# Kernel tuning notes

Hardware: AMD Instinct MI355X
Metric: run time of the kernel (lower is better)

## Reference

```python
import jax, jax.numpy as jnp
import numpy as np

T, H, F, E, K = 1024, 1024, 2048, 8, 2  # tokens, hidden, ffn_inter, experts, top_k


def setup_inputs() -> dict:
    key = jax.random.key(0)
    ks = jax.random.split(key, 7)
    return {
        "hidden_states": jax.random.normal(ks[0], (T, H), dtype=jnp.float32),
        "token_selected_experts": jax.random.randint(ks[1], (T, K), 0, E, dtype=jnp.int32),
        "token_final_scales": jax.random.uniform(ks[2], (T, K), dtype=jnp.float32),
        "w1": jax.random.normal(ks[3], (E, 2 * F, H), dtype=jnp.float32) * 0.02,  # gated fc1: [gate; linear]
        "b1": jax.random.normal(ks[4], (E, 2 * F), dtype=jnp.float32) * 0.02,
        "w2": jax.random.normal(ks[5], (E, H, F), dtype=jnp.float32) * 0.02,
        "b2": jax.random.normal(ks[6], (E, H), dtype=jnp.float32) * 0.02,
    }


def reference(hidden_states, token_selected_experts, token_final_scales, w1, b1, w2, b2):
    # Grouped GEMM fc1 over all experts: [T, E, 2F]
    h1 = jnp.einsum('th,efh->tef', hidden_states, w1) + b1[None]
    ffn = w2.shape[2]
    gate, lin = h1[..., :ffn], h1[..., ffn:]
    act = jax.nn.silu(gate) * lin                      # swiglu gated activation, [T, E, F]
    y_all = jnp.einsum('tef,ehf->teh', act, w2) + b2[None]  # fc2, [T, E, H]
    # Gather the top-k selected experts per token and combine with final scales
    sel = token_selected_experts.astype(jnp.int32)     # [T, K]
    y_sel = jnp.take_along_axis(y_all, sel[:, :, None], axis=1)  # [T, K, H]
    out = jnp.sum(y_sel * token_final_scales[:, :, None], axis=1)  # [T, H]
    return out
```

## Files before the change

### kernel.cpp

```cpp
#include <hip/hip_runtime.h>
#include <hip/hip_bf16.h>
#include <cstdint>
#include <cstddef>

#define TDIM 1024
#define HDIM 1024
#define FDIM 2048
#define NEXP 8
#define NENT 2048

typedef __bf16 bf16_t;
typedef __bf16 bf16x4 __attribute__((ext_vector_type(4)));
typedef __bf16 bf16x8 __attribute__((ext_vector_type(8)));
typedef float  f32x4  __attribute__((ext_vector_type(4)));

#define H_ELEMS ((size_t)TDIM*HDIM)

#define WB_OFFSETS 0
#define WB_ETOK    64
#define WB_ESCALE  (WB_ETOK + NENT*4)
#define WB_ACT     16512
#define WB_H       (WB_ACT + (size_t)NENT*FDIM*2)

__device__ __forceinline__ void gload16(const void* g, void* l) {
  __builtin_amdgcn_global_load_lds((const __attribute__((address_space(1))) void*)g,
                                   (__attribute__((address_space(3))) void*)l, 16, 0, 0);
}

__global__ void route_all(const int* __restrict__ sel, const float* __restrict__ scal,
                          int* __restrict__ offsets, int* __restrict__ etok,
                          float* __restrict__ escale) {
  __shared__ int cnt[NEXP], cnt2[NEXP], offs[NEXP+1];
  const int t = threadIdx.x;
  if (t < NEXP) { cnt[t] = 0; cnt2[t] = 0; }
  __syncthreads();
  int e8[8];
  #pragma unroll
  for (int q = 0; q < 8; q++) {
    int i = t*8 + q;
    e8[q] = sel[i];
    atomicAdd(&cnt[e8[q]], 1);
  }
  __syncthreads();
  if (t == 0) {
    int s = 0;
    for (int e = 0; e < NEXP; e++) { offs[e] = s; offsets[e] = s; s += cnt[e]; }
    offs[NEXP] = s; offsets[NEXP] = s;
  }
  __syncthreads();
  #pragma unroll
  for (int q = 0; q < 8; q++) {
    int i = t*8 + q;
    int e = e8[q];
    int pos = offs[e] + atomicAdd(&cnt2[e], 1);
    etok[pos]   = i >> 1;
    escale[pos] = scal[i];
  }
}

__global__ void convert_h(const float* __restrict__ h, bf16_t* __restrict__ hbf) {
  size_t idx = ((size_t)blockIdx.x*256 + threadIdx.x) * 8;
  float4 v0 = ((const float4*)(h + idx))[0];
  float4 v1 = ((const float4*)(h + idx))[1];
  bf16x8 o;
  o[0]=(bf16_t)v0.x; o[1]=(bf16_t)v0.y; o[2]=(bf16_t)v0.z; o[3]=(bf16_t)v0.w;
  o[4]=(bf16_t)v1.x; o[5]=(bf16_t)v1.y; o[6]=(bf16_t)v1.z; o[7]=(bf16_t)v1.w;
  *(bf16x8*)(hbf + idx) = o;
}


__global__ __launch_bounds__(512, 4) void gemm1_v3(
    const bf16_t* __restrict__ hbf, const float* __restrict__ w1,
    const float* __restrict__ b1, const int* __restrict__ offsets,
    const int* __restrict__ etok, bf16_t* __restrict__ act)
{
  const int e   = blockIdx.z;
  const int off = offsets[e];
  const int nt  = offsets[e+1] - off;
  const int m0  = blockIdx.y * 128;
  if (m0 >= nt) return;
  const int n0  = blockIdx.x * 64;

  __shared__ __align__(16) bf16_t As[2][128*32];
  __shared__ __align__(16) bf16_t Bg[64*32];
  __shared__ __align__(16) bf16_t Bl[64*32];

  const int tid  = threadIdx.x;
  const int w    = tid >> 6, lane = tid & 63;
  const int quad = lane >> 4, lr = lane & 15;
  const int wm   = w >> 1,  wn = w & 1;

  const int ar   = w*16 + (lane >> 2);
  const int aseg = (lane & 3) ^ (ar & 3);
  int ent = m0 + ar; if (ent > nt-1) ent = nt-1;
  const int tok = etok[off + ent];
  const bf16_t* asrc = hbf + (size_t)tok*HDIM + aseg*8;
  bf16_t* adst[2] = { &As[0][w*512], &As[1][w*512] };

  const int tr = tid >> 3, c4 = tid & 7;
  const float* gsrc = w1 + ((size_t)e*2*FDIM + (size_t)(n0 + tr))*HDIM + c4*4;
  const float* lsrc = gsrc + (size_t)FDIM*HDIM;
  const int bofs = tr*32 + (((c4 >> 1) ^ (tr & 3)) << 3) + (c4 & 1)*4;

  f32x4 accg[2][2] = {}, accl[2][2] = {};

  gload16(asrc, adst[0]);
  float4 g4 = *(const float4*)gsrc;
  float4 l4 = *(const float4*)lsrc;

  int p = 0;
  for (int k0 = 0; k0 < HDIM; k0 += 32, p ^= 1) {
    __syncthreads();
    {
      bf16x4 v;
      v[0]=(bf16_t)g4.x; v[1]=(bf16_t)g4.y; v[2]=(bf16_t)g4.z; v[3]=(bf16_t)g4.w;
      *(bf16x4*)&Bg[bofs] = v;
      v[0]=(bf16_t)l4.x; v[1]=(bf16_t)l4.y; v[2]=(bf16_t)l4.z; v[3]=(bf16_t)l4.w;
      *(bf16x4*)&Bl[bofs] = v;
    }
    if (k0 + 32 < HDIM) {
      gload16(asrc + k0 + 32, adst[p^1]);
      g4 = *(const float4*)(gsrc + k0 + 32);
      l4 = *(const float4*)(lsrc + k0 + 32);
    }
    __syncthreads();

    bf16x8 af[2], gf[2], lf[2];
    #pragma unroll
    for (int i = 0; i < 2; i++) {
      const int m = wm*32 + i*16 + lr;
      af[i] = *(const bf16x8*)&As[p][m*32 + ((quad ^ (m & 3)) << 3)];
    }
    #pragma unroll
    for (int j = 0; j < 2; j++) {
      const int n = wn*32 + j*16 + lr;
      gf[j] = *(const bf16x8*)&Bg[n*32 + ((quad ^ (n & 3)) << 3)];
      lf[j] = *(const bf16x8*)&Bl[n*32 + ((quad ^ (n & 3)) << 3)];
    }
    #pragma unroll
    for (int i = 0; i < 2; i++)
      #pragma unroll
      for (int j = 0; j < 2; j++) {
        accg[i][j] = __builtin_amdgcn_mfma_f32_16x16x32_bf16(af[i], gf[j], accg[i][j], 0, 0, 0);
        accl[i][j] = __builtin_amdgcn_mfma_f32_16x16x32_bf16(af[i], lf[j], accl[i][j], 0, 0, 0);
      }
  }

  #pragma unroll
  for (int j = 0; j < 2; j++) {
    const int f = n0 + wn*32 + j*16 + lr;
    const float bg_ = b1[e*2*FDIM + f];
    const float bl_ = b1[e*2*FDIM + FDIM + f];
    #pragma unroll
    for (int i = 0; i < 2; i++) {
      #pragma unroll
      for (int r = 0; r < 4; r++) {
        const int m = wm*32 + i*16 + quad*4 + r;
        if (m0 + m < nt) {
          const float g = accg[i][j][r] + bg_;
          const float l = accl[i][j][r] + bl_;
          const float s = g / (1.f + __expf(-g)) * l;
          act[(size_t)(off + m0 + m)*FDIM + f] = (bf16_t)s;
        }
      }
    }
  }
}

__global__ __launch_bounds__(512, 4) void gemm2_v3(
    const bf16_t* __restrict__ act, const float* __restrict__ w2,
    const float* __restrict__ b2, const int* __restrict__ offsets,
    const int* __restrict__ etok, const float* __restrict__ escale,
    float* __restrict__ out)
{
  const int e   = blockIdx.z;
  const int off = offsets[e];
  const int nt  = offsets[e+1] - off;
  const int m0  = blockIdx.y * 128;
  if (m0 >= nt) return;
  const int n0  = (blockIdx.x >> 1) * 64;
  const int kc  = blockIdx.x & 1;
  const int kbeg = kc * (FDIM/2);

  __shared__ __align__(16) bf16_t As[2][128*32];
  __shared__ __align__(16) bf16_t Bs[64*32];

  const int tid  = threadIdx.x;
  const int w    = tid >> 6, lane = tid & 63;
  const int quad = lane >> 4, lr = lane & 15;
  const int wm   = w >> 1,  wn = w & 1;

  const int ar   = w*16 + (lane >> 2);
  const int aseg = (lane & 3) ^ (ar & 3);
  int ent = m0 + ar; if (ent > nt-1) ent = nt-1;
  const bf16_t* asrc = act + (size_t)(off + ent)*FDIM + kbeg + aseg*8;
  bf16_t* adst[2] = { &As[0][w*512], &As[1][w*512] };

  const int tr = tid >> 3, c4 = tid & 7;
  const float* bsrc = w2 + ((size_t)e*HDIM + (size_t)(n0 + tr))*FDIM + kbeg + c4*4;
  const int bofs = tr*32 + (((c4 >> 1) ^ (tr & 3)) << 3) + (c4 & 1)*4;

  f32x4 acc[2][2] = {};

  gload16(asrc, adst[0]);
  float4 b4 = *(const float4*)bsrc;

  int p = 0;
  for (int k0 = 0; k0 < FDIM/2; k0 += 32, p ^= 1) {
    __syncthreads();
    {
      bf16x4 v;
      v[0]=(bf16_t)b4.x; v[1]=(bf16_t)b4.y; v[2]=(bf16_t)b4.z; v[3]=(bf16_t)b4.w;
      *(bf16x4*)&Bs[bofs] = v;
    }
    if (k0 + 32 < FDIM/2) {
      gload16(asrc + k0 + 32, adst[p^1]);
      b4 = *(const float4*)(bsrc + k0 + 32);
    }
    __syncthreads();

    bf16x8 af[2], bfr[2];
    #pragma unroll
    for (int i = 0; i < 2; i++) {
      const int m = wm*32 + i*16 + lr;
      af[i] = *(const bf16x8*)&As[p][m*32 + ((quad ^ (m & 3)) << 3)];
    }
    #pragma unroll
    for (int j = 0; j < 2; j++) {
      const int n = wn*32 + j*16 + lr;
      bfr[j] = *(const bf16x8*)&Bs[n*32 + ((quad ^ (n & 3)) << 3)];
    }
    #pragma unroll
    for (int i = 0; i < 2; i++)
      #pragma unroll
      for (int j = 0; j < 2; j++)
        acc[i][j] = __builtin_amdgcn_mfma_f32_16x16x32_bf16(af[i], bfr[j], acc[i][j], 0, 0, 0);
  }

  #pragma unroll
  for (int i = 0; i < 2; i++) {
    #pragma unroll
    for (int r = 0; r < 4; r++) {
      const int m = wm*32 + i*16 + quad*4 + r;
      if (m0 + m < nt) {
        const int slot = off + m0 + m;
        const int t    = etok[slot];
        const float s  = escale[slot];
        #pragma unroll
        for (int j = 0; j < 2; j++) {
          const int n = n0 + wn*32 + j*16 + lr;
          float v = acc[i][j][r];
          if (kc == 0) v += b2[e*HDIM + n];
          atomicAdd(&out[(size_t)t*HDIM + n], s * v);
        }
      }
    }
  }
}

extern "C" void kernel_launch(void* const* d_in, const int* in_sizes, int n_in,
                              void* d_out, int out_size, void* d_ws, size_t ws_size,
                              hipStream_t stream) {
  const float* hidden = (const float*)d_in[0];
  const int*   sel    = (const int*)d_in[1];
  const float* scal   = (const float*)d_in[2];
  const float* w1     = (const float*)d_in[3];
  const float* b1     = (const float*)d_in[4];
  const float* w2     = (const float*)d_in[5];
  const float* b2     = (const float*)d_in[6];
  float* out = (float*)d_out;

  char* ws = (char*)d_ws;
  int*    offsets = (int*)(ws + WB_OFFSETS);
  int*    etok    = (int*)(ws + WB_ETOK);
  float*  escale  = (float*)(ws + WB_ESCALE);
  bf16_t* act     = (bf16_t*)(ws + WB_ACT);
  bf16_t* hbf     = (bf16_t*)(ws + WB_H);

  hipMemsetAsync(d_out, 0, (size_t)out_size * sizeof(float), stream);

  route_all<<<1, 256, 0, stream>>>(sel, scal, offsets, etok, escale);
  convert_h<<<(int)(H_ELEMS/8/256), 256, 0, stream>>>(hidden, hbf);

  gemm1_v3<<<dim3(FDIM/64, NENT/128, NEXP), 512, 0, stream>>>(hbf, w1, b1, offsets, etok, act);
  gemm2_v3<<<dim3((HDIM/64)*2, NENT/128, NEXP), 512, 0, stream>>>(act, w2, b2, offsets, etok, escale, out);
}
```

Before: 346.6 us.

## Drop LDS staging in MoE GEMMs and load MFMA fragments directly from global

Both grouped GEMM kernels stop staging A and B tiles through shared memory. Each lane now reads its MFMA fragments straight from global memory and converts fp32 weights to bf16 in registers. The M tile shrinks from 128 to 64 rows and blocks from 512 to 256 threads, so more blocks launch. This removes the barriers and LDS traffic, but loses cross-wave reuse: each wave re-reads weights and activations from global, and a lane's 32-byte row slices are not coalesced, so memory traffic goes up.

```diff
diff --git a/kernel.cpp b/kernel.cpp
--- a/kernel.cpp
+++ b/kernel.cpp
@@ -21,11 +21,6 @@
 #define WB_ESCALE  (WB_ETOK + NENT*4)
 #define WB_ACT     16512
 #define WB_H       (WB_ACT + (size_t)NENT*FDIM*2)
-
-__device__ __forceinline__ void gload16(const void* g, void* l) {
-  __builtin_amdgcn_global_load_lds((const __attribute__((address_space(1))) void*)g,
-                                   (__attribute__((address_space(3))) void*)l, 16, 0, 0);
-}
 
 __global__ void route_all(const int* __restrict__ sel, const float* __restrict__ scal,
                           int* __restrict__ offsets, int* __restrict__ etok,
@@ -68,8 +63,15 @@
   *(bf16x8*)(hbf + idx) = o;
 }
 
-
-__global__ __launch_bounds__(512, 4) void gemm1_v3(
+__device__ __forceinline__ bf16x8 cvt8(const float4 a, const float4 b) {
+  bf16x8 o;
+  o[0]=(bf16_t)a.x; o[1]=(bf16_t)a.y; o[2]=(bf16_t)a.z; o[3]=(bf16_t)a.w;
+  o[4]=(bf16_t)b.x; o[5]=(bf16_t)b.y; o[6]=(bf16_t)b.z; o[7]=(bf16_t)b.w;
+  return o;
+}
+
+
+__global__ __launch_bounds__(256, 4) void gemm1_v4(
     const bf16_t* __restrict__ hbf, const float* __restrict__ w1,
     const float* __restrict__ b1, const int* __restrict__ offsets,
     const int* __restrict__ etok, bf16_t* __restrict__ act)
@@ -77,65 +79,47 @@
   const int e   = blockIdx.z;
   const int off = offsets[e];
   const int nt  = offsets[e+1] - off;
-  const int m0  = blockIdx.y * 128;
+  const int m0  = blockIdx.y * 64;
   if (m0 >= nt) return;
   const int n0  = blockIdx.x * 64;
-
-  __shared__ __align__(16) bf16_t As[2][128*32];
-  __shared__ __align__(16) bf16_t Bg[64*32];
-  __shared__ __align__(16) bf16_t Bl[64*32];
 
   const int tid  = threadIdx.x;
   const int w    = tid >> 6, lane = tid & 63;
   const int quad = lane >> 4, lr = lane & 15;
   const int wm   = w >> 1,  wn = w & 1;
 
-  const int ar   = w*16 + (lane >> 2);
-  const int aseg = (lane & 3) ^ (ar & 3);
-  int ent = m0 + ar; if (ent > nt-1) ent = nt-1;
-  const int tok = etok[off + ent];
-  const bf16_t* asrc = hbf + (size_t)tok*HDIM + aseg*8;
-  bf16_t* adst[2] = { &As[0][w*512], &As[1][w*512] };
-
-  const int tr = tid >> 3, c4 = tid & 7;
-  const float* gsrc = w1 + ((size_t)e*2*FDIM + (size_t)(n0 + tr))*HDIM + c4*4;
-  const float* lsrc = gsrc + (size_t)FDIM*HDIM;
-  const int bofs = tr*32 + (((c4 >> 1) ^ (tr & 3)) << 3) + (c4 & 1)*4;
+  const bf16_t* aptr[2];
+  #pragma unroll
+  for (int i = 0; i < 2; i++) {
+    int ent = m0 + wm*32 + i*16 + lr;
+    if (ent > nt-1) ent = nt-1;
+    const int tok = etok[off + ent];
+    aptr[i] = hbf + (size_t)tok*HDIM + quad*8;
+  }
+  const float* gptr[2];
+  const float* lptr[2];
+  #pragma unroll
+  for (int j = 0; j < 2; j++) {
+    const int n = n0 + wn*32 + j*16 + lr;
+    gptr[j] = w1 + ((size_t)e*2*FDIM + n)*HDIM + quad*8;
+    lptr[j] = gptr[j] + (size_t)FDIM*HDIM;
+  }
 
   f32x4 accg[2][2] = {}, accl[2][2] = {};
 
-  gload16(asrc, adst[0]);
-  float4 g4 = *(const float4*)gsrc;
-  float4 l4 = *(const float4*)lsrc;
-
-  int p = 0;
-  for (int k0 = 0; k0 < HDIM; k0 += 32, p ^= 1) {
-    __syncthreads();
-    {
-      bf16x4 v;
-      v[0]=(bf16_t)g4.x; v[1]=(bf16_t)g4.y; v[2]=(bf16_t)g4.z; v[3]=(bf16_t)g4.w;
-      *(bf16x4*)&Bg[bofs] = v;
-      v[0]=(bf16_t)l4.x; v[1]=(bf16_t)l4.y; v[2]=(bf16_t)l4.z; v[3]=(bf16_t)l4.w;
-      *(bf16x4*)&Bl[bofs] = v;
-    }
-    if (k0 + 32 < HDIM) {
-      gload16(asrc + k0 + 32, adst[p^1]);
-      g4 = *(const float4*)(gsrc + k0 + 32);
-      l4 = *(const float4*)(lsrc + k0 + 32);
-    }
-    __syncthreads();
-
+  for (int k0 = 0; k0 < HDIM; k0 += 32) {
     bf16x8 af[2], gf[2], lf[2];
     #pragma unroll
-    for (int i = 0; i < 2; i++) {
-      const int m = wm*32 + i*16 + lr;
-      af[i] = *(const bf16x8*)&As[p][m*32 + ((quad ^ (m & 3)) << 3)];
-    }
+    for (int i = 0; i < 2; i++)
+      af[i] = *(const bf16x8*)(aptr[i] + k0);
     #pragma unroll
     for (int j = 0; j < 2; j++) {
-      const int n = wn*32 + j*16 + lr;
-      gf[j] = *(const bf16x8*)&Bg[n*32 + ((quad ^ (n & 3)) << 3)];
-      lf[j] = *(const bf16x8*)&Bl[n*32 + ((quad ^ (n & 3)) << 3)];
+      const float4* gp = (const float4*)(gptr[j] + k0);
+      const float4* lp = (const float4*)(lptr[j] + k0);
+      float4 ga = gp[0], gb = gp[1];
+      float4 la = lp[0], lb = lp[1];
+      gf[j] = cvt8(ga, gb);
+      lf[j] = cvt8(la, lb);
     }
     #pragma unroll
     for (int i = 0; i < 2; i++)
@@ -167,7 +151,7 @@
   }
 }
 
-__global__ __launch_bounds__(512, 4) void gemm2_v3(
+__global__ __launch_bounds__(256, 4) void gemm2_v4(
     const bf16_t* __restrict__ act, const float* __restrict__ w2,
     const float* __restrict__ b2, const int* __restrict__ offsets,
     const int* __restrict__ etok, const float* __restrict__ escale,
@@ -176,59 +160,43 @@
   const int e   = blockIdx.z;
   const int off = offsets[e];
   const int nt  = offsets[e+1] - off;
-  const int m0  = blockIdx.y * 128;
+  const int m0  = blockIdx.y * 64;
   if (m0 >= nt) return;
   const int n0  = (blockIdx.x >> 1) * 64;
   const int kc  = blockIdx.x & 1;
   const int kbeg = kc * (FDIM/2);
 
-  __shared__ __align__(16) bf16_t As[2][128*32];
-  __shared__ __align__(16) bf16_t Bs[64*32];
-
   const int tid  = threadIdx.x;
   const int w    = tid >> 6, lane = tid & 63;
   const int quad = lane >> 4, lr = lane & 15;
   const int wm   = w >> 1,  wn = w & 1;
 
-  const int ar   = w*16 + (lane >> 2);
-  const int aseg = (lane & 3) ^ (ar & 3);
-  int ent = m0 + ar; if (ent > nt-1) ent = nt-1;
-  const bf16_t* asrc = act + (size_t)(off + ent)*FDIM + kbeg + aseg*8;
-  bf16_t* adst[2] = { &As[0][w*512], &As[1][w*512] };
-
-  const int tr = tid >> 3, c4 = tid & 7;
-  const float* bsrc = w2 + ((size_t)e*HDIM + (size_t)(n0 + tr))*FDIM + kbeg + c4*4;
-  const int bofs = tr*32 + (((c4 >> 1) ^ (tr & 3)) << 3) + (c4 & 1)*4;
+  const bf16_t* aptr[2];
+  #pragma unroll
+  for (int i = 0; i < 2; i++) {
+    int ent = m0 + wm*32 + i*16 + lr;
+    if (ent > nt-1) ent = nt-1;
+    aptr[i] = act + (size_t)(off + ent)*FDIM + kbeg + quad*8;
+  }
+  const float* bptr[2];
+  #pragma unroll
+  for (int j = 0; j < 2; j++) {
+    const int n = n0 + wn*32 + j*16 + lr;
+    bptr[j] = w2 + ((size_t)e*HDIM + n)*FDIM + kbeg + quad*8;
+  }
 
   f32x4 acc[2][2] = {};
 
-  gload16(asrc, adst[0]);
-  float4 b4 = *(const float4*)bsrc;
-
-  int p = 0;
-  for (int k0 = 0; k0 < FDIM/2; k0 += 32, p ^= 1) {
-    __syncthreads();
-    {
-      bf16x4 v;
-      v[0]=(bf16_t)b4.x; v[1]=(bf16_t)b4.y; v[2]=(bf16_t)b4.z; v[3]=(bf16_t)b4.w;
-      *(bf16x4*)&Bs[bofs] = v;
-    }
-    if (k0 + 32 < FDIM/2) {
-      gload16(asrc + k0 + 32, adst[p^1]);
-      b4 = *(const float4*)(bsrc + k0 + 32);
-    }
-    __syncthreads();
-
+  for (int k0 = 0; k0 < FDIM/2; k0 += 32) {
     bf16x8 af[2], bfr[2];
     #pragma unroll
-    for (int i = 0; i < 2; i++) {
-      const int m = wm*32 + i*16 + lr;
-      af[i] = *(const bf16x8*)&As[p][m*32 + ((quad ^ (m & 3)) << 3)];
-    }
+    for (int i = 0; i < 2; i++)
+      af[i] = *(const bf16x8*)(aptr[i] + k0);
     #pragma unroll
     for (int j = 0; j < 2; j++) {
-      const int n = wn*32 + j*16 + lr;
-      bfr[j] = *(const bf16x8*)&Bs[n*32 + ((quad ^ (n & 3)) << 3)];
+      const float4* bp = (const float4*)(bptr[j] + k0);
+      float4 ba = bp[0], bb = bp[1];
+      bfr[j] = cvt8(ba, bb);
     }
     #pragma unroll
     for (int i = 0; i < 2; i++)
@@ -282,6 +250,6 @@
   route_all<<<1, 256, 0, stream>>>(sel, scal, offsets, etok, escale);
   convert_h<<<(int)(H_ELEMS/8/256), 256, 0, stream>>>(hidden, hbf);
 
-  gemm1_v3<<<dim3(FDIM/64, NENT/128, NEXP), 512, 0, stream>>>(hbf, w1, b1, offsets, etok, act);
-  gemm2_v3<<<dim3((HDIM/64)*2, NENT/128, NEXP), 512, 0, stream>>>(act, w2, b2, offsets, etok, escale, out);
-}
+  gemm1_v4<<<dim3(FDIM/64, NENT/64, NEXP), 256, 0, stream>>>(hbf, w1, b1, offsets, etok, act);
+  gemm2_v4<<<dim3((HDIM/64)*2, NENT/64, NEXP), 256, 0, stream>>>(act, w2, b2, offsets, etok, escale, out);
+}
```

Result: slower. 574.8 us (+65.8%).
